# Kernel tuning notes

Measured on AMD Instinct MI355X. Metric: run time of the kernel, lower is better.

The kernel has to match this reference:

```python
import jax, jax.numpy as jnp
import numpy as np

EPS = 1e-5

def _bn_train(x, gamma, beta):
    # BatchNorm2d in training mode: batch stats over (N,H,W), biased variance
    mean = jnp.mean(x, axis=(0, 2, 3), keepdims=True)
    var = jnp.mean((x - mean) ** 2, axis=(0, 2, 3), keepdims=True)
    xn = (x - mean) / jnp.sqrt(var + EPS)
    return xn * gamma[None, :, None, None] + beta[None, :, None, None]

def _bin_act(x):
    # forward: sign(x); backward: grad of clamp(x,-1,1) (STE)
    c = jnp.clip(x, -1.0, 1.0)
    return jax.lax.stop_gradient(jnp.sign(x) - c) + c

def _bin_conv(x, w_flat, out_chn, in_chn, k=3, stride=1, padding=1):
    w = w_flat.reshape(out_chn, in_chn, k, k)
    scale = jax.lax.stop_gradient(jnp.mean(jnp.abs(w), axis=(1, 2, 3), keepdims=True))
    cw = jnp.clip(w, -1.0, 1.0)
    bw = jax.lax.stop_gradient(scale * jnp.sign(w) - cw) + cw
    return jax.lax.conv_general_dilated(
        x, bw, window_strides=(stride, stride),
        padding=[(padding, padding), (padding, padding)],
        dimension_numbers=('NCHW', 'OIHW', 'NCHW'))

def _prelu(x, a):
    return jnp.where(x >= 0, x, a * x)

def setup_inputs() -> dict:
    key = jax.random.key(0)
    ks = jax.random.split(key, 4)
    C = 128
    x = jax.random.normal(ks[0], (64, C, 56, 56), dtype=jnp.float32)
    # HardBinaryConv stores weights as (n,1); init small, mixed-sign
    w1 = (jax.random.uniform(ks[1], (C * C * 9, 1), dtype=jnp.float32) - 0.5) * 0.002
    w2 = (jax.random.uniform(ks[2], (C * C * 9, 1), dtype=jnp.float32) - 0.5) * 0.002
    ones = jnp.ones((C,), jnp.float32)
    zeros = jnp.zeros((C,), jnp.float32)
    a = jnp.float32(0.25)
    return {
        'x': x,
        'bn1_g': ones, 'bn1_b': zeros,
        'w1': w1, 'prelu1_a': a,
        'bn2_g': ones, 'bn2_b': zeros,
        'w2': w2, 'prelu2_a': a,
        'bn3_g': ones, 'bn3_b': zeros,
        'prelu3_a': a,
    }

def reference(x, bn1_g, bn1_b, w1, prelu1_a, bn2_g, bn2_b, w2, prelu2_a, bn3_g, bn3_b, prelu3_a):
    C = x.shape[1]
    out = _bn_train(x, bn1_g, bn1_b)
    out = _bin_act(out)
    out = _prelu(_bin_conv(out, w1, C, C), prelu1_a)
    out = _bn_train(out, bn2_g, bn2_b)
    out = _bin_act(out)
    out = _bin_conv(out, w2, C, C)
    out = _prelu(out, prelu2_a)
    out = _bn_train(out, bn3_g, bn3_b)
    out = out + x  # identity shortcut (stride=1, in_planes==planes)
    out = _prelu(out, prelu3_a)
    return out
```

## Files before the change

### kernel.cpp

```cpp
#include <hip/hip_runtime.h>
#include <hip/hip_bf16.h>

typedef __attribute__((ext_vector_type(8))) short short8;
typedef __attribute__((ext_vector_type(4))) int i32x4;

#define HW     3136
#define M_TOT  200704
#define NSTEP  18
#define NBLK   784

__device__ __forceinline__ void gload_lds16(const void* g, void* l) {
    __builtin_amdgcn_global_load_lds(
        (const __attribute__((address_space(1))) void*)g,
        (__attribute__((address_space(3))) void*)l, 16, 0, 0);
}

__global__ __launch_bounds__(256) void wsign_kernel(const float* __restrict__ w1,
                                                    const float* __restrict__ w2,
                                                    char* __restrict__ ws1,
                                                    char* __restrict__ ws2) {
    int i = blockIdx.x * 256 + threadIdx.x;
    const float* w = w1;
    char* wsz = ws1;
    if (i >= 147456) { i -= 147456; w = w2; wsz = ws2; }
    int e = i & 15, l = (i >> 4) & 63, f = (i >> 10) & 7, s = i >> 13;
    int cout = f * 16 + (l & 15);
    int k = s * 64 + (l >> 4) * 16 + e;
    int tap = k >> 7, cin = k & 127;
    float v = w[(cout * 128 + cin) * 9 + tap];
    wsz[i] = v > 0.f ? (char)1 : (v < 0.f ? (char)-1 : (char)0);
}

__global__ __launch_bounds__(256) void wscale_kernel(const float* __restrict__ w1,
                                                     const float* __restrict__ w2,
                                                     float* __restrict__ scale1,
                                                     float* __restrict__ scale2) {
    int o = blockIdx.x;
    const float* w = w1;
    float* scale = scale1;
    if (o >= 128) { o -= 128; w = w2; scale = scale2; }
    int t = threadIdx.x;
    float s = 0.f;
    for (int i = t; i < 1152; i += 256) s += fabsf(w[o * 1152 + i]);
    __shared__ float r1[256];
    r1[t] = s; __syncthreads();
    for (int off = 128; off > 0; off >>= 1) {
        if (t < off) r1[t] += r1[t + off];
        __syncthreads();
    }
    if (t == 0) scale[o] = r1[0] * (1.f / 1152.f);
}

__global__ __launch_bounds__(256) void stats_nchw_kernel(const float* __restrict__ x,
                                                         float* __restrict__ psum,
                                                         float* __restrict__ psq) {
    int bid = blockIdx.x;
    int n = bid >> 7, c = bid & 127;
    const float* p = x + (n * 128 + c) * HW;
    int t = threadIdx.x;
    float s = 0.f, q = 0.f;
    for (int i = t; i < HW; i += 256) { float v = p[i]; s += v; q += v * v; }
    __shared__ float r1[256], r2[256];
    r1[t] = s; r2[t] = q; __syncthreads();
    for (int off = 128; off > 0; off >>= 1) {
        if (t < off) { r1[t] += r1[t + off]; r2[t] += r2[t + off]; }
        __syncthreads();
    }
    if (t == 0) { psum[c * 64 + n] = r1[0]; psq[c * 64 + n] = r2[0]; }
}

__global__ void finalize_kernel(const float* __restrict__ psum, const float* __restrict__ psq,
                                int P, float* __restrict__ mean, float* __restrict__ rstd) {
    int c = threadIdx.x;
    if (c >= 128) return;
    float s = 0.f, q = 0.f;
    for (int j = 0; j < P; ++j) { s += psum[c * P + j]; q += psq[c * P + j]; }
    const float invN = 1.f / 200704.f;
    float m = s * invN;
    float var = q * invN - m * m;
    mean[c] = m;
    rstd[c] = 1.f / sqrtf(var + 1e-5f);
}

__global__ __launch_bounds__(256) void finalizeB_kernel(const float* __restrict__ psumB,
                                                        const float* __restrict__ psqB,
                                                        float* __restrict__ mean,
                                                        float* __restrict__ rstd) {
    int c = blockIdx.x, t = threadIdx.x;
    float s = 0.f, q = 0.f;
    for (int j = t; j < NBLK; j += 256) { s += psumB[c * NBLK + j]; q += psqB[c * NBLK + j]; }
    __shared__ float r1[256], r2[256];
    r1[t] = s; r2[t] = q; __syncthreads();
    for (int off = 128; off > 0; off >>= 1) {
        if (t < off) { r1[t] += r1[t + off]; r2[t] += r2[t + off]; }
        __syncthreads();
    }
    if (t == 0) {
        const float invN = 1.f / 200704.f;
        float m = r1[0] * invN;
        float var = r2[0] * invN - m * m;
        mean[c] = m;
        rstd[c] = 1.f / sqrtf(var + 1e-5f);
    }
}

__global__ __launch_bounds__(256) void act1_kernel(const float* __restrict__ x,
        const float* __restrict__ mean, const float* __restrict__ rstd,
        const float* __restrict__ g, const float* __restrict__ b,
        char* __restrict__ apad) {
    __shared__ float row[128 * 57];
    int blk = blockIdx.x;
    int n = blk / 58, hp = blk - n * 58;
    char* o = apad + (n * 58 + hp) * 58 * 128;
    int t = threadIdx.x;
    if (hp == 0 || hp == 57) {
        for (int i4 = t; i4 < 58 * 32; i4 += 256)
            *(char4*)(o + i4 * 4) = make_char4(0, 0, 0, 0);
        return;
    }
    const float* src = x + n * (128 * HW) + (hp - 1) * 56;
    for (int i = t; i < 128 * 56; i += 256) {
        int c = i / 56, w = i - c * 56;
        row[c * 57 + w] = src[c * HW + w];
    }
    __syncthreads();
    for (int i4 = t; i4 < 58 * 32; i4 += 256) {
        int wp = i4 >> 5;
        int c0 = (i4 & 31) * 4;
        char q[4] = {0, 0, 0, 0};
        if (wp >= 1 && wp <= 56) {
#pragma unroll
            for (int k = 0; k < 4; ++k) {
                int c = c0 + k;
                float xn = (row[c * 57 + wp - 1] - mean[c]) * rstd[c] * g[c] + b[c];
                q[k] = xn > 0.f ? 1 : (xn < 0.f ? -1 : 0);
            }
        }
        *(char4*)(o + wp * 128 + c0) = make_char4(q[0], q[1], q[2], q[3]);
    }
}

__global__ __launch_bounds__(256) void act2_kernel(const short* __restrict__ p1,
        const float* __restrict__ scale1, const float* __restrict__ a1ptr,
        const float* __restrict__ mean, const float* __restrict__ rstd,
        const float* __restrict__ g, const float* __restrict__ b,
        char* __restrict__ apad) {
    __shared__ float row[128 * 57];
    int blk = blockIdx.x;
    int n = blk / 58, hp = blk - n * 58;
    char* o = apad + (n * 58 + hp) * 58 * 128;
    int t = threadIdx.x;
    if (hp == 0 || hp == 57) {
        for (int i4 = t; i4 < 58 * 32; i4 += 256)
            *(char4*)(o + i4 * 4) = make_char4(0, 0, 0, 0);
        return;
    }
    float a1 = a1ptr[0];
    const short* src = p1 + n * HW + (hp - 1) * 56;
    for (int i = t; i < 128 * 56; i += 256) {
        int c = i / 56, w = i - c * 56;
        float v = scale1[c] * (float)src[(size_t)c * M_TOT + w];
        row[c * 57 + w] = v >= 0.f ? v : a1 * v;
    }
    __syncthreads();
    for (int i4 = t; i4 < 58 * 32; i4 += 256) {
        int wp = i4 >> 5;
        int c0 = (i4 & 31) * 4;
        char q[4] = {0, 0, 0, 0};
        if (wp >= 1 && wp <= 56) {
#pragma unroll
            for (int k = 0; k < 4; ++k) {
                int c = c0 + k;
                float xn = (row[c * 57 + wp - 1] - mean[c]) * rstd[c] * g[c] + b[c];
                q[k] = xn > 0.f ? 1 : (xn < 0.f ? -1 : 0);
            }
        }
        *(char4*)(o + wp * 128 + c0) = make_char4(q[0], q[1], q[2], q[3]);
    }
}

__global__ __launch_bounds__(512, 4) void conv_kernel(
        const char* __restrict__ apad,
        const char* __restrict__ wswz,
        const float* __restrict__ scale,
        const float* __restrict__ aptr,
        short* __restrict__ obuf,
        float* __restrict__ psumB,
        float* __restrict__ psqB) {
    __shared__ __align__(1024) char lds[3][24576];
    __shared__ float partS[512];
    __shared__ float partQ[512];

    const int tid = threadIdx.x;
    const int lane = tid & 63;
    const int wid = tid >> 6;
    const int l15 = lane & 15;
    const int lq = lane >> 4;
    const int wr = wid >> 2;
    const int wc = wid & 3;

    int bid = blockIdx.x;
    int mblk = (bid & 7) * 98 + (bid >> 3);
    const int m0 = mblk * 256;

    const char* bsrc[2];
#pragma unroll
    for (int j = 0; j < 2; ++j) {
        int m = m0 + (j * 8 + wid) * 16 + l15;
        int n = m / HW;
        int r = m - n * HW;
        int h = r / 56;
        int w = r - h * 56;
        bsrc[j] = apad + (((n * 58 + h) * 58 + w) * 128 + lq * 16);
    }

    i32x4 acc[4][4];
#pragma unroll
    for (int i = 0; i < 4; ++i)
#pragma unroll
        for (int j = 0; j < 4; ++j)
            acc[i][j] = (i32x4){0, 0, 0, 0};

    auto stage = [&](int s, int buf) {
        int tap = s >> 1;
        int dh = tap / 3;
        int dw = tap - dh * 3;
        int toff = (dh * 58 + dw) * 128 + (s & 1) * 64;
        gload_lds16(wswz + s * 8192 + tid * 16, lds[buf] + wid * 1024);
        gload_lds16(bsrc[0] + toff, lds[buf] + 8192 + wid * 1024);
        gload_lds16(bsrc[1] + toff, lds[buf] + 16384 + wid * 1024);
    };

    stage(0, 0);
    stage(1, 1);

    for (int s = 0; s < NSTEP; ++s) {
        if (s + 1 < NSTEP) asm volatile("s_waitcnt vmcnt(3)" ::: "memory");
        else               asm volatile("s_waitcnt vmcnt(0)" ::: "memory");
        __builtin_amdgcn_s_barrier();
        __builtin_amdgcn_sched_barrier(0);
        if (s + 2 < NSTEP) stage(s + 2, (s + 2) % 3);

        const char* buf = lds[s % 3];
        i32x4 af[4], bf[4];
#pragma unroll
        for (int ci = 0; ci < 4; ++ci)
            af[ci] = *(const i32x4*)(buf + (wr * 4 + ci) * 1024 + lane * 16);
#pragma unroll
        for (int mi = 0; mi < 4; ++mi)
            bf[mi] = *(const i32x4*)(buf + 8192 + (wc * 4 + mi) * 1024 + lane * 16);
#pragma unroll
        for (int ci = 0; ci < 4; ++ci)
#pragma unroll
            for (int mi = 0; mi < 4; ++mi)
                acc[ci][mi] = __builtin_amdgcn_mfma_i32_16x16x64_i8(
                    af[ci], bf[mi], acc[ci][mi], 0, 0, 0);
    }

    float alpha = aptr[0];
#pragma unroll
    for (int ci = 0; ci < 4; ++ci) {
        int cb = wr * 64 + ci * 16 + lq * 4;
        int mb = m0 + wc * 64 + l15;
#pragma unroll
        for (int r = 0; r < 4; ++r) {
            float sc = scale[cb + r];
            short* op = obuf + (size_t)(cb + r) * M_TOT + mb;
            float s = 0.f, q = 0.f;
#pragma unroll
            for (int mi = 0; mi < 4; ++mi) {
                int iv = acc[ci][mi][r];
                float v = (float)iv * sc;
                float pv = v >= 0.f ? v : alpha * v;
                op[mi * 16] = (short)iv;
                s += pv; q += pv * pv;
            }
#pragma unroll
            for (int msk = 1; msk <= 8; msk <<= 1) {
                s += __shfl_xor(s, msk, 64);
                q += __shfl_xor(q, msk, 64);
            }
            if (l15 == 0) { partS[wc * 128 + cb + r] = s; partQ[wc * 128 + cb + r] = q; }
        }
    }
    __syncthreads();
    if (tid < 128) {
        psumB[tid * NBLK + bid] = partS[tid] + partS[128 + tid] + partS[256 + tid] + partS[384 + tid];
        psqB [tid * NBLK + bid] = partQ[tid] + partQ[128 + tid] + partQ[256 + tid] + partQ[384 + tid];
    }
}

__global__ __launch_bounds__(256) void final_kernel(const short* __restrict__ p2,
        const float* __restrict__ scale2, const float* __restrict__ a2ptr,
        const float* __restrict__ x,
        const float* __restrict__ mean, const float* __restrict__ rstd,
        const float* __restrict__ g, const float* __restrict__ b,
        const float* __restrict__ a3ptr, float* __restrict__ out) {
    int bid = blockIdx.x;
    int n = bid >> 7, c = bid & 127;
    float sc = scale2[c], a2 = a2ptr[0];
    float m = mean[c], r = rstd[c], gg = g[c], bb = b[c], a3 = a3ptr[0];
    const short* pp = p2 + (size_t)c * M_TOT + n * HW;
    const float* xx = x + (n * 128 + c) * HW;
    float* oo = out + (n * 128 + c) * HW;
    int t = threadIdx.x;
    for (int i8 = t; i8 < 392; i8 += 256) {
        short8 v = *(const short8*)(pp + i8 * 8);
        float4 x0 = *(const float4*)(xx + i8 * 8);
        float4 x1 = *(const float4*)(xx + i8 * 8 + 4);
        float o[8];
#pragma unroll
        for (int k = 0; k < 8; ++k) {
            float pv = (float)v[k] * sc;
            pv = pv >= 0.f ? pv : a2 * pv;
            float xv = (k < 4) ? ((const float*)&x0)[k] : ((const float*)&x1)[k - 4];
            float val = (pv - m) * r * gg + bb + xv;
            o[k] = val >= 0.f ? val : a3 * val;
        }
        *(float4*)(oo + i8 * 8)     = make_float4(o[0], o[1], o[2], o[3]);
        *(float4*)(oo + i8 * 8 + 4) = make_float4(o[4], o[5], o[6], o[7]);
    }
}

extern "C" void kernel_launch(void* const* d_in, const int* in_sizes, int n_in,
                              void* d_out, int out_size, void* d_ws, size_t ws_size,
                              hipStream_t stream) {
    const float* x  = (const float*)d_in[0];
    const float* g1 = (const float*)d_in[1];
    const float* b1 = (const float*)d_in[2];
    const float* w1 = (const float*)d_in[3];
    const float* a1 = (const float*)d_in[4];
    const float* g2 = (const float*)d_in[5];
    const float* b2 = (const float*)d_in[6];
    const float* w2 = (const float*)d_in[7];
    const float* a2 = (const float*)d_in[8];
    const float* g3 = (const float*)d_in[9];
    const float* b3 = (const float*)d_in[10];
    const float* a3 = (const float*)d_in[11];
    float* out = (float*)d_out;
    char* ws = (char*)d_ws;

    float* scale1 = (float*)(ws);
    float* scale2 = (float*)(ws + 512);
    float* mean1  = (float*)(ws + 1024);
    float* rstd1  = (float*)(ws + 1536);
    float* mean2  = (float*)(ws + 2048);
    float* rstd2  = (float*)(ws + 2560);
    float* mean3  = (float*)(ws + 3072);
    float* rstd3  = (float*)(ws + 3584);
    float* psum   = (float*)(ws + 4096);
    float* psq    = (float*)(ws + 36864);
    float* psumB  = (float*)(ws + 69632);
    float* psqB   = (float*)(ws + 872448);
    char* wswz1   = (char*)(ws + 1675264);
    char* wswz2   = (char*)(ws + 1822720);
    char* apad8   = (char*)(ws + 1970176);
    short* buf2s  = (short*)(ws + 29528064);
    short* buf1s  = (short*)out;

    wscale_kernel<<<256, 256, 0, stream>>>(w1, w2, scale1, scale2);
    wsign_kernel<<<1152, 256, 0, stream>>>(w1, w2, wswz1, wswz2);

    stats_nchw_kernel<<<8192, 256, 0, stream>>>(x, psum, psq);
    finalize_kernel<<<1, 128, 0, stream>>>(psum, psq, 64, mean1, rstd1);
    act1_kernel<<<3712, 256, 0, stream>>>(x, mean1, rstd1, g1, b1, apad8);
    conv_kernel<<<NBLK, 512, 0, stream>>>(apad8, wswz1, scale1, a1, buf1s, psumB, psqB);

    finalizeB_kernel<<<128, 256, 0, stream>>>(psumB, psqB, mean2, rstd2);
    act2_kernel<<<3712, 256, 0, stream>>>(buf1s, scale1, a1, mean2, rstd2, g2, b2, apad8);
    conv_kernel<<<NBLK, 512, 0, stream>>>(apad8, wswz2, scale2, a2, buf2s, psumB, psqB);

    finalizeB_kernel<<<128, 256, 0, stream>>>(psumB, psqB, mean3, rstd3);
    final_kernel<<<8192, 256, 0, stream>>>(buf2s, scale2, a2, x, mean3, rstd3, g3, b3, a3, out);
}
```

Baseline: 273.4 us.

## Halve conv M-tile, use full-tap K stages with XOR-swizzled activation LDS layout

Restructures the int8 MFMA conv kernel. Each block now covers 128 output pixels instead of 256, so twice as many blocks run. Each pipeline stage loads a full 3x3 tap covering all 128 input channels (9 iterations instead of 18 half-tap steps), and the weight swizzle kernel is reordered to match. Activation rows are stored in LDS with an XOR swizzle to avoid bank conflicts, s_setprio is raised around the MFMA block, and the reduction scratch now reuses the pipeline LDS. In exchange, each block does half the weight reuse, uses more LDS per block, and the launch bound drops to 2 blocks, which may lower occupancy.

```diff
diff --git a/kernel.cpp b/kernel.cpp
--- a/kernel.cpp
+++ b/kernel.cpp
@@ -6,8 +6,8 @@
 
 #define HW     3136
 #define M_TOT  200704
-#define NSTEP  18
-#define NBLK   784
+#define NITER  9
+#define NBLK   1568
 
 __device__ __forceinline__ void gload_lds16(const void* g, void* l) {
     __builtin_amdgcn_global_load_lds(
@@ -23,11 +23,10 @@
     const float* w = w1;
     char* wsz = ws1;
     if (i >= 147456) { i -= 147456; w = w2; wsz = ws2; }
-    int e = i & 15, l = (i >> 4) & 63, f = (i >> 10) & 7, s = i >> 13;
+    int e = i & 15, l = (i >> 4) & 63, f = (i >> 10) & 7, ks = (i >> 13) & 1, t = i >> 14;
     int cout = f * 16 + (l & 15);
-    int k = s * 64 + (l >> 4) * 16 + e;
-    int tap = k >> 7, cin = k & 127;
-    float v = w[(cout * 128 + cin) * 9 + tap];
+    int cin = ks * 64 + (l >> 4) * 16 + e;
+    float v = w[(cout * 128 + cin) * 9 + t];
     wsz[i] = v > 0.f ? (char)1 : (v < 0.f ? (char)-1 : (char)0);
 }
 
@@ -179,7 +178,7 @@
     }
 }
 
-__global__ __launch_bounds__(512, 4) void conv_kernel(
+__global__ __launch_bounds__(512, 2) void conv_kernel(
         const char* __restrict__ apad,
         const char* __restrict__ wswz,
         const float* __restrict__ scale,
@@ -187,9 +186,7 @@
         short* __restrict__ obuf,
         float* __restrict__ psumB,
         float* __restrict__ psqB) {
-    __shared__ __align__(1024) char lds[3][24576];
-    __shared__ float partS[512];
-    __shared__ float partQ[512];
+    __shared__ __align__(1024) char lds[3][32768];
 
     const int tid = threadIdx.x;
     const int lane = tid & 63;
@@ -200,75 +197,92 @@
     const int wc = wid & 3;
 
     int bid = blockIdx.x;
-    int mblk = (bid & 7) * 98 + (bid >> 3);
-    const int m0 = mblk * 256;
+    int mblk = (bid & 7) * 196 + (bid >> 3);
+    const int m0 = mblk * 128;
 
     const char* bsrc[2];
-#pragma unroll
-    for (int j = 0; j < 2; ++j) {
-        int m = m0 + (j * 8 + wid) * 16 + l15;
-        int n = m / HW;
-        int r = m - n * HW;
-        int h = r / 56;
-        int w = r - h * 56;
-        bsrc[j] = apad + (((n * 58 + h) * 58 + w) * 128 + lq * 16);
-    }
-
-    i32x4 acc[4][4];
+    {
+        int kb = (tid & 7) * 16;
+#pragma unroll
+        for (int j = 0; j < 2; ++j) {
+            int mloc = j * 64 + (tid >> 3);
+            int m = m0 + mloc;
+            int n = m / HW;
+            int r = m - n * HW;
+            int h = r / 56;
+            int w = r - h * 56;
+            bsrc[j] = apad + (((n * 58 + h) * 58 + w) * 128 + (kb ^ ((mloc & 7) << 4)));
+        }
+    }
+
+    i32x4 acc[4][2];
 #pragma unroll
     for (int i = 0; i < 4; ++i)
 #pragma unroll
-        for (int j = 0; j < 4; ++j)
+        for (int j = 0; j < 2; ++j)
             acc[i][j] = (i32x4){0, 0, 0, 0};
 
-    auto stage = [&](int s, int buf) {
-        int tap = s >> 1;
-        int dh = tap / 3;
-        int dw = tap - dh * 3;
-        int toff = (dh * 58 + dw) * 128 + (s & 1) * 64;
-        gload_lds16(wswz + s * 8192 + tid * 16, lds[buf] + wid * 1024);
-        gload_lds16(bsrc[0] + toff, lds[buf] + 8192 + wid * 1024);
-        gload_lds16(bsrc[1] + toff, lds[buf] + 16384 + wid * 1024);
+    auto stage = [&](int t, int buf) {
+        int dh = t / 3;
+        int dw = t - dh * 3;
+        int toff = (dh * 58 + dw) * 128;
+        const char* wsrc = wswz + t * 16384 + tid * 16;
+        gload_lds16(wsrc,        lds[buf] + wid * 1024);
+        gload_lds16(wsrc + 8192, lds[buf] + 8192 + wid * 1024);
+        gload_lds16(bsrc[0] + toff, lds[buf] + 16384 + wid * 1024);
+        gload_lds16(bsrc[1] + toff, lds[buf] + 24576 + wid * 1024);
     };
 
     stage(0, 0);
     stage(1, 1);
 
-    for (int s = 0; s < NSTEP; ++s) {
-        if (s + 1 < NSTEP) asm volatile("s_waitcnt vmcnt(3)" ::: "memory");
+    for (int t = 0; t < NITER; ++t) {
+        if (t + 1 < NITER) asm volatile("s_waitcnt vmcnt(4)" ::: "memory");
         else               asm volatile("s_waitcnt vmcnt(0)" ::: "memory");
         __builtin_amdgcn_s_barrier();
         __builtin_amdgcn_sched_barrier(0);
-        if (s + 2 < NSTEP) stage(s + 2, (s + 2) % 3);
-
-        const char* buf = lds[s % 3];
-        i32x4 af[4], bf[4];
+        if (t + 2 < NITER) stage(t + 2, (t + 2) % 3);
+
+        const char* bufp = lds[t % 3];
+        i32x4 af[4][2], bf[2][2];
+#pragma unroll
+        for (int ks = 0; ks < 2; ++ks) {
+#pragma unroll
+            for (int ci = 0; ci < 4; ++ci)
+                af[ci][ks] = *(const i32x4*)(bufp + ks * 8192 + (wr * 4 + ci) * 1024 + lane * 16);
+#pragma unroll
+            for (int mi = 0; mi < 2; ++mi) {
+                int mloc = wc * 32 + mi * 16 + l15;
+                int kbyte = (ks * 64 + lq * 16) ^ ((mloc & 7) << 4);
+                bf[mi][ks] = *(const i32x4*)(bufp + 16384 + mloc * 128 + kbyte);
+            }
+        }
+        __builtin_amdgcn_s_setprio(1);
 #pragma unroll
         for (int ci = 0; ci < 4; ++ci)
-            af[ci] = *(const i32x4*)(buf + (wr * 4 + ci) * 1024 + lane * 16);
-#pragma unroll
-        for (int mi = 0; mi < 4; ++mi)
-            bf[mi] = *(const i32x4*)(buf + 8192 + (wc * 4 + mi) * 1024 + lane * 16);
-#pragma unroll
-        for (int ci = 0; ci < 4; ++ci)
-#pragma unroll
-            for (int mi = 0; mi < 4; ++mi)
-                acc[ci][mi] = __builtin_amdgcn_mfma_i32_16x16x64_i8(
-                    af[ci], bf[mi], acc[ci][mi], 0, 0, 0);
+#pragma unroll
+            for (int mi = 0; mi < 2; ++mi)
+#pragma unroll
+                for (int ks = 0; ks < 2; ++ks)
+                    acc[ci][mi] = __builtin_amdgcn_mfma_i32_16x16x64_i8(
+                        af[ci][ks], bf[mi][ks], acc[ci][mi], 0, 0, 0);
+        __builtin_amdgcn_s_setprio(0);
     }
 
     float alpha = aptr[0];
+    float* partS = (float*)&lds[0][0];
+    float* partQ = (float*)&lds[0][2048];
 #pragma unroll
     for (int ci = 0; ci < 4; ++ci) {
         int cb = wr * 64 + ci * 16 + lq * 4;
-        int mb = m0 + wc * 64 + l15;
+        int mb = m0 + wc * 32 + l15;
 #pragma unroll
         for (int r = 0; r < 4; ++r) {
             float sc = scale[cb + r];
             short* op = obuf + (size_t)(cb + r) * M_TOT + mb;
             float s = 0.f, q = 0.f;
 #pragma unroll
-            for (int mi = 0; mi < 4; ++mi) {
+            for (int mi = 0; mi < 2; ++mi) {
                 int iv = acc[ci][mi][r];
                 float v = (float)iv * sc;
                 float pv = v >= 0.f ? v : alpha * v;
```

Result: slower. 300.2 us (+9.8%).
